# Kernel tuning notes

Hardware: AMD Instinct MI355X
Metric: run time of the kernel (lower is better)

## Reference

```python
import jax, jax.numpy as jnp
import numpy as np

N_NODES = 100000
N_EDGES = 1600000
IN_DIM, HID_DIM, OUT_DIM = 128, 256, 128


def gcn_conv(x, src, dst, W, b, n):
    # PyG GCNConv: linear transform, add self-loops, symmetric normalization,
    # scatter-sum aggregation over destination nodes, then bias.
    h = x @ W  # [n, d_out]
    loops = jnp.arange(n, dtype=src.dtype)
    s = jnp.concatenate([src, loops])
    d = jnp.concatenate([dst, loops])
    deg = jax.ops.segment_sum(jnp.ones_like(d, dtype=h.dtype), d, num_segments=n)
    dinv = jnp.where(deg > 0, jax.lax.rsqrt(deg), 0.0)
    norm = dinv[s] * dinv[d]  # [E+n]
    msg = h[s] * norm[:, None]  # gather + scale
    out = jax.ops.segment_sum(msg, d, num_segments=n)  # scatter-reduce
    return out + b


def layer_norm(x, gamma, beta, eps=1e-5):
    mu = jnp.mean(x, axis=-1, keepdims=True)
    var = jnp.mean(jnp.square(x - mu), axis=-1, keepdims=True)
    return (x - mu) * jax.lax.rsqrt(var + eps) * gamma + beta


def setup_inputs() -> dict:
    key = jax.random.key(0)
    ks = jax.random.split(key, 8)
    x = jax.random.normal(ks[0], (N_NODES, IN_DIM), dtype=jnp.float32)
    edge_index = jax.random.randint(ks[1], (2, N_EDGES), 0, N_NODES, dtype=jnp.int64)
    W1 = jax.random.normal(ks[2], (IN_DIM, HID_DIM), dtype=jnp.float32) * (1.0 / np.sqrt(IN_DIM))
    b1 = jnp.zeros((HID_DIM,), dtype=jnp.float32)
    W2 = jax.random.normal(ks[3], (HID_DIM, OUT_DIM), dtype=jnp.float32) * (1.0 / np.sqrt(HID_DIM))
    b2 = jnp.zeros((OUT_DIM,), dtype=jnp.float32)
    gamma = jnp.ones((OUT_DIM,), dtype=jnp.float32)
    beta = jnp.zeros((OUT_DIM,), dtype=jnp.float32)
    return {"x": x, "edge_index": edge_index, "W1": W1, "b1": b1,
            "W2": W2, "b2": b2, "gamma": gamma, "beta": beta}


def reference(x, edge_index, W1, b1, W2, b2, gamma, beta):
    n = x.shape[0]
    src, dst = edge_index[0], edge_index[1]
    h = gcn_conv(x, src, dst, W1, b1, n)
    h = jax.nn.relu(h)
    # dropout(p=0.1) is identity in eval mode
    h = gcn_conv(h, src, dst, W2, b2, n)
    return layer_norm(h, gamma, beta)
```

## Files before the change

kernel.cpp:

```cpp
#include <hip/hip_runtime.h>
#include <hip/hip_fp16.h>
#include <stdint.h>

#define N_NODES 100000
#define N_EDGES 1600000
#define IN_DIM  128
#define HID_DIM 256
#define OUT_DIM 128
#define RS 264
#define NBUCK 391
#define EPB   4096
#define PADB  5120
#define PB    391
#define WB    256

typedef __attribute__((ext_vector_type(8))) _Float16 f16x8;
typedef __attribute__((ext_vector_type(4))) float f32x4;

__device__ __forceinline__ int clampi(int v) {
    v = v < 0 ? 0 : v;
    return v >= N_NODES ? N_NODES - 1 : v;
}
__device__ __forceinline__ float2 h2f2(uint32_t u) {
    union { uint32_t u; __half2 h; } c; c.u = u;
    return __half22float2(c.h);
}
__device__ __forceinline__ uint32_t packh(float a, float b) {
    union { __half2 h; uint32_t u; } c; c.h = __floats2half2_rn(a, b);
    return c.u;
}
__device__ __forceinline__ uint16_t f2h(float a) {
    union { __half h; uint16_t s; } c; c.h = __float2half_rn(a);
    return c.s;
}

__device__ __forceinline__ int src_at(const int* ei, int isI64, int e) {
    return clampi(isI64 ? ei[2 * (size_t)e] : ei[e]);
}
__device__ __forceinline__ int dst_at(const int* ei, int isI64, int e) {
    return clampi(isI64 ? ei[2 * (size_t)N_EDGES + 2 * (size_t)e]
                        : ei[(size_t)N_EDGES + e]);
}


__global__ __launch_bounds__(256) void partition_kernel(const int* __restrict__ ei,
                                                        int* __restrict__ cursor,
                                                        uint2* __restrict__ recs,
                                                        const float* __restrict__ W1,
                                                        uint16_t* __restrict__ W1t,
                                                        const float* __restrict__ W2,
                                                        uint16_t* __restrict__ W2t) {
    if (blockIdx.x >= PB) {
        int idx = (blockIdx.x - PB) * 256 + threadIdx.x;
        if (idx < IN_DIM * HID_DIM) {
            int k = idx / HID_DIM, n = idx - k * HID_DIM;
            W1t[n * IN_DIM + k] = f2h(W1[idx]);
        } else {
            int j = idx - IN_DIM * HID_DIM;
            int k = j / OUT_DIM, n = j - k * OUT_DIM;
            W2t[n * HID_DIM + k] = f2h(W2[j]);
        }
        return;
    }
    __shared__ int hist[NBUCK];
    __shared__ int histBase[NBUCK];
    __shared__ int gBase[NBUCK];
    __shared__ int scanT[512];
    __shared__ uint2 lrec[EPB];
    __shared__ int s_flag;
    int tid = threadIdx.x;
    if (tid == 0) {
        int z = 1;
        #pragma unroll
        for (int i = 0; i < 16; ++i)
            if (ei[2 * i + 1] != 0) z = 0;
        s_flag = z;
    }
    for (int b = tid; b < NBUCK; b += 256) hist[b] = 0;
    __syncthreads();
    int isI64 = s_flag;
    int base = blockIdx.x * EPB;
    int srcs[16], dsts[16], slots[16];
    #pragma unroll
    for (int r = 0; r < 16; ++r) {
        int e = base + r * 256 + tid;
        slots[r] = -1;
        srcs[r] = 0; dsts[r] = 0;
        if (e < N_EDGES) {
            srcs[r] = src_at(ei, isI64, e);
            dsts[r] = dst_at(ei, isI64, e);
            slots[r] = atomicAdd(&hist[dsts[r] >> 8], 1);
        }
    }
    __syncthreads();
    scanT[tid]       = (tid < NBUCK) ? hist[tid] : 0;
    scanT[tid + 256] = (tid + 256 < NBUCK) ? hist[tid + 256] : 0;
    __syncthreads();
    for (int off = 1; off < 512; off <<= 1) {
        int v0 = (tid >= off) ? scanT[tid - off] : 0;
        int v1 = scanT[tid + 256 - off];
        __syncthreads();
        if (tid >= off) scanT[tid] += v0;
        scanT[tid + 256] += v1;
        __syncthreads();
    }
    for (int b = tid; b < NBUCK; b += 256) {
        histBase[b] = b ? scanT[b - 1] : 0;
        if (hist[b] > 0) gBase[b] = atomicAdd(&cursor[b], hist[b]);
    }
    __syncthreads();
    #pragma unroll
    for (int r = 0; r < 16; ++r) {
        if (slots[r] >= 0) {
            int b = dsts[r] >> 8;
            uint2 rec; rec.x = (unsigned)srcs[r]; rec.y = (unsigned)dsts[r];
            lrec[histBase[b] + slots[r]] = rec;
        }
    }
    __syncthreads();
    int nvalid = N_EDGES - base; if (nvalid > EPB) nvalid = EPB;
    for (int i = tid; i < nvalid; i += 256) {
        uint2 rec = lrec[i];
        int b = (int)(rec.y >> 8);
        int pos = gBase[b] + (i - histBase[b]);
        if (pos < PADB)
            recs[(size_t)b * PADB + pos] = rec;
    }
}


__global__ __launch_bounds__(256) void build_kernel(const uint2* __restrict__ recs,
                                                    const int* __restrict__ cursor,
                                                    int* __restrict__ row_ptr,
                                                    float* __restrict__ dinv,
                                                    int* __restrict__ colv,
                                                    const float* __restrict__ x,
                                                    uint2* __restrict__ xsout) {
    __shared__ uint2 lrec[PADB];
    __shared__ int cnt[256];
    __shared__ int lofs[256];
    __shared__ int cur[256];
    __shared__ int scanT[256];
    int b = blockIdx.x, tid = threadIdx.x;
    int nb = cursor[b]; if (nb > PADB) nb = PADB;
    int pv = 0;
    for (int j = tid; j < b; j += 256) {
        int c = cursor[j];
        pv += (c > PADB) ? PADB : c;
    }
    cnt[tid] = 0; cur[tid] = 0;
    scanT[tid] = pv;
    __syncthreads();
    for (int off = 128; off > 0; off >>= 1) {
        if (tid < off) scanT[tid] += scanT[tid + off];
        __syncthreads();
    }
    int cbase = scanT[0];
    __syncthreads();
    for (int i = tid; i < nb; i += 256) {
        uint2 r = recs[(size_t)b * PADB + i];
        lrec[i] = r;
        atomicAdd(&cnt[r.y & 255], 1);
    }
    __syncthreads();
    scanT[tid] = cnt[tid];
    __syncthreads();
    for (int off = 1; off < 256; off <<= 1) {
        int x2 = (tid >= off) ? scanT[tid - off] : 0;
        __syncthreads();
        if (tid >= off) scanT[tid] += x2;
        __syncthreads();
    }
    lofs[tid] = tid ? scanT[tid - 1] : 0;
    int node = b * 256 + tid;
    if (node < N_NODES) {
        row_ptr[node] = cbase + lofs[tid];
        dinv[node] = rsqrtf((float)(cnt[tid] + 1));
    }
    if (b == NBUCK - 1 && tid == 0) row_ptr[N_NODES] = cbase + nb;
    __syncthreads();
    for (int i = tid; i < nb; i += 256) {
        uint2 r = lrec[i];
        int id = (int)(r.y & 255);
        int slot = atomicAdd(&cur[id], 1);
        colv[cbase + lofs[id] + slot] = (int)r.x;
    }
    const float4* x4 = (const float4*)x + (size_t)b * 8192;
    uint2* xo = xsout + (size_t)b * 8192;
    int lim = (N_NODES - b * 256) * 32; if (lim > 8192) lim = 8192;
    for (int j = tid; j < lim; j += 256) {
        float d = rsqrtf((float)(cnt[j >> 5] + 1));
        float4 v = x4[j];
        uint2 o;
        o.x = packh(d * v.x, d * v.y);
        o.y = packh(d * v.z, d * v.w);
        xo[j] = o;
    }
}


template<bool LN>
__global__ __launch_bounds__(256) void agg_kernel(const uint4* __restrict__ rows,
                                                  const int* __restrict__ row_ptr,
                                                  const int* __restrict__ colv,
                                                  const float* __restrict__ dinv,
                                                  const float* __restrict__ bias,
                                                  const float* __restrict__ gamma,
                                                  const float* __restrict__ beta,
                                                  float* __restrict__ out,
                                                  uint4* __restrict__ out16) {
    int node = blockIdx.x * 16 + (threadIdx.x >> 4);
    if (node >= N_NODES) return;
    int l = threadIdx.x & 15;
    const char* base = (const char*)rows + ((unsigned)l << 4);
    float di = dinv[node];
    float acc[8];
    {
        uint4 u = *(const uint4*)(base + ((unsigned)node << 8));
        float2 f0 = h2f2(u.x), f1 = h2f2(u.y), f2 = h2f2(u.z), f3 = h2f2(u.w);
        acc[0] = f0.x; acc[1] = f0.y; acc[2] = f1.x; acc[3] = f1.y;
        acc[4] = f2.x; acc[5] = f2.y; acc[6] = f3.x; acc[7] = f3.y;
    }
    int e = row_ptr[node], e1 = row_ptr[node + 1];
    int s0 = 0, s1 = 0, s2 = 0, s3 = 0;
    if (e     < e1) s0 = colv[e];
    if (e + 1 < e1) s1 = colv[e + 1];
    if (e + 2 < e1) s2 = colv[e + 2];
    if (e + 3 < e1) s3 = colv[e + 3];
    while (e + 4 <= e1) {
        uint4 v0 = *(const uint4*)(base + ((unsigned)s0 << 8));
        uint4 v1 = *(const uint4*)(base + ((unsigned)s1 << 8));
        uint4 v2 = *(const uint4*)(base + ((unsigned)s2 << 8));
        uint4 v3 = *(const uint4*)(base + ((unsigned)s3 << 8));
        int p0 = (e + 4 < e1) ? e + 4 : e;
        int p1 = (e + 5 < e1) ? e + 5 : e;
        int p2 = (e + 6 < e1) ? e + 6 : e;
        int p3 = (e + 7 < e1) ? e + 7 : e;
        int t0 = colv[p0], t1 = colv[p1], t2 = colv[p2], t3 = colv[p3];
        {
            float2 f0 = h2f2(v0.x), f1 = h2f2(v0.y), f2 = h2f2(v0.z), f3 = h2f2(v0.w);
            acc[0] += f0.x; acc[1] += f0.y; acc[2] += f1.x; acc[3] += f1.y;
            acc[4] += f2.x; acc[5] += f2.y; acc[6] += f3.x; acc[7] += f3.y;
        }
        {
            float2 f0 = h2f2(v1.x), f1 = h2f2(v1.y), f2 = h2f2(v1.z), f3 = h2f2(v1.w);
            acc[0] += f0.x; acc[1] += f0.y; acc[2] += f1.x; acc[3] += f1.y;
            acc[4] += f2.x; acc[5] += f2.y; acc[6] += f3.x; acc[7] += f3.y;
        }
        {
            float2 f0 = h2f2(v2.x), f1 = h2f2(v2.y), f2 = h2f2(v2.z), f3 = h2f2(v2.w);
            acc[0] += f0.x; acc[1] += f0.y; acc[2] += f1.x; acc[3] += f1.y;
            acc[4] += f2.x; acc[5] += f2.y; acc[6] += f3.x; acc[7] += f3.y;
        }
        {
            float2 f0 = h2f2(v3.x), f1 = h2f2(v3.y), f2 = h2f2(v3.z), f3 = h2f2(v3.w);
            acc[0] += f0.x; acc[1] += f0.y; acc[2] += f1.x; acc[3] += f1.y;
            acc[4] += f2.x; acc[5] += f2.y; acc[6] += f3.x; acc[7] += f3.y;
        }
        s0 = t0; s1 = t1; s2 = t2; s3 = t3; e += 4;
    }
    int r = e1 - e;
    if (r > 0) {
        uint4 v = *(const uint4*)(base + ((unsigned)s0 << 8));
        float2 f0 = h2f2(v.x), f1 = h2f2(v.y), f2 = h2f2(v.z), f3 = h2f2(v.w);
        acc[0] += f0.x; acc[1] += f0.y; acc[2] += f1.x; acc[3] += f1.y;
        acc[4] += f2.x; acc[5] += f2.y; acc[6] += f3.x; acc[7] += f3.y;
    }
    if (r > 1) {
        uint4 v = *(const uint4*)(base + ((unsigned)s1 << 8));
        float2 f0 = h2f2(v.x), f1 = h2f2(v.y), f2 = h2f2(v.z), f3 = h2f2(v.w);
        acc[0] += f0.x; acc[1] += f0.y; acc[2] += f1.x; acc[3] += f1.y;
        acc[4] += f2.x; acc[5] += f2.y; acc[6] += f3.x; acc[7] += f3.y;
    }
    if (r > 2) {
        uint4 v = *(const uint4*)(base + ((unsigned)s2 << 8));
        float2 f0 = h2f2(v.x), f1 = h2f2(v.y), f2 = h2f2(v.z), f3 = h2f2(v.w);
        acc[0] += f0.x; acc[1] += f0.y; acc[2] += f1.x; acc[3] += f1.y;
        acc[4] += f2.x; acc[5] += f2.y; acc[6] += f3.x; acc[7] += f3.y;
    }
    if (!LN) {
        uint4 o;
        o.x = packh(acc[0] * di, acc[1] * di);
        o.y = packh(acc[2] * di, acc[3] * di);
        o.z = packh(acc[4] * di, acc[5] * di);
        o.w = packh(acc[6] * di, acc[7] * di);
        out16[(size_t)node * 16 + l] = o;
    } else {
        const float4* b4 = (const float4*)(bias + l * 8);
        float4 bb0 = b4[0], bb1 = b4[1];
        float v[8];
        v[0] = acc[0] * di + bb0.x; v[1] = acc[1] * di + bb0.y;
        v[2] = acc[2] * di + bb0.z; v[3] = acc[3] * di + bb0.w;
        v[4] = acc[4] * di + bb1.x; v[5] = acc[5] * di + bb1.y;
        v[6] = acc[6] * di + bb1.z; v[7] = acc[7] * di + bb1.w;
        float s = 0.f;
        #pragma unroll
        for (int j = 0; j < 8; ++j) s += v[j];
        #pragma unroll
        for (int o = 8; o > 0; o >>= 1) s += __shfl_xor(s, o, 64);
        float mu = s * (1.0f / 128.0f);
        float q = 0.f;
        #pragma unroll
        for (int j = 0; j < 8; ++j) { v[j] -= mu; q += v[j] * v[j]; }
        #pragma unroll
        for (int o = 8; o > 0; o >>= 1) q += __shfl_xor(q, o, 64);
        float rstd = rsqrtf(q * (1.0f / 128.0f) + 1e-5f);
        const float4* g4 = (const float4*)(gamma + l * 8);
        const float4* t4 = (const float4*)(beta + l * 8);
        float4 g0 = g4[0], g1 = g4[1], t0 = t4[0], t1 = t4[1];
        float* orow = out + (size_t)node * 128 + l * 8;
        f32x4 o0, o1;
        o0.x = v[0] * rstd * g0.x + t0.x; o0.y = v[1] * rstd * g0.y + t0.y;
        o0.z = v[2] * rstd * g0.z + t0.z; o0.w = v[3] * rstd * g0.w + t0.w;
        o1.x = v[4] * rstd * g1.x + t1.x; o1.y = v[5] * rstd * g1.y + t1.y;
        o1.z = v[6] * rstd * g1.z + t1.z; o1.w = v[7] * rstd * g1.w + t1.w;
        __builtin_nontemporal_store(o0, (f32x4*)orow);
        __builtin_nontemporal_store(o1, (f32x4*)(orow + 4));
    }
}


__global__ __launch_bounds__(256) void fused_gemm_kernel(const uint16_t* __restrict__ A16,
                                                         const uint16_t* __restrict__ W1t,
                                                         const float* __restrict__ b1,
                                                         const uint16_t* __restrict__ W2t,
                                                         const float* __restrict__ dinv,
                                                         uint16_t* __restrict__ G16, int M) {
    __shared__ __align__(16) uint16_t Hs[64 * RS];
    int lane = threadIdx.x & 63;
    int wave = threadIdx.x >> 6;
    int r15 = lane & 15;
    int quad = lane >> 4;
    int kofs = quad * 8;
    int blk_row = blockIdx.x * 64;

    f16x8 a[4][4];
    #pragma unroll
    for (int mt = 0; mt < 4; ++mt) {
        bool valid = (blk_row + mt * 16) < M;
        int row = valid ? (blk_row + mt * 16 + r15) : 0;
        const uint16_t* arow = A16 + (size_t)row * IN_DIM + kofs;
        #pragma unroll
        for (int ks = 0; ks < 4; ++ks)
            a[mt][ks] = *(const f16x8*)(arow + ks * 32);
    }

    #pragma unroll
    for (int nt = 0; nt < 4; ++nt) {
        int ncol = (wave * 4 + nt) * 16 + r15;
        const uint16_t* bp = W1t + (size_t)ncol * IN_DIM + kofs;
        f32x4 acc[4];
        #pragma unroll
        for (int mt = 0; mt < 4; ++mt) acc[mt] = (f32x4){0.f, 0.f, 0.f, 0.f};
        #pragma unroll
        for (int ks = 0; ks < 4; ++ks) {
            f16x8 bv = *(const f16x8*)(bp + ks * 32);
            #pragma unroll
            for (int mt = 0; mt < 4; ++mt)
                acc[mt] = __builtin_amdgcn_mfma_f32_16x16x32_f16(a[mt][ks], bv, acc[mt], 0, 0, 0);
        }
        float bb = b1[ncol];
        #pragma unroll
        for (int mt = 0; mt < 4; ++mt) {
            #pragma unroll
            for (int r = 0; r < 4; ++r) {
                int lrow = mt * 16 + quad * 4 + r;
                Hs[lrow * RS + ncol] = f2h(fmaxf(acc[mt][r] + bb, 0.f));
            }
        }
    }
    __syncthreads();

    #pragma unroll
    for (int nt = 0; nt < 2; ++nt) {
        int ncol = (wave * 2 + nt) * 16 + r15;
        const uint16_t* bp = W2t + (size_t)ncol * HID_DIM + kofs;
        f16x8 b2[8];
        #pragma unroll
        for (int ks = 0; ks < 8; ++ks)
            b2[ks] = *(const f16x8*)(bp + ks * 32);
        f32x4 acc[4];
        #pragma unroll
        for (int mt = 0; mt < 4; ++mt) acc[mt] = (f32x4){0.f, 0.f, 0.f, 0.f};
        #pragma unroll
        for (int ks = 0; ks < 8; ++ks) {
            #pragma unroll
            for (int mt = 0; mt < 4; ++mt) {
                f16x8 av = *(const f16x8*)(Hs + (mt * 16 + r15) * RS + ks * 32 + kofs);
                acc[mt] = __builtin_amdgcn_mfma_f32_16x16x32_f16(av, b2[ks], acc[mt], 0, 0, 0);
            }
        }
        #pragma unroll
        for (int mt = 0; mt < 4; ++mt) {
            if ((blk_row + mt * 16) < M) {
                #pragma unroll
                for (int r = 0; r < 4; ++r) {
                    int row = blk_row + mt * 16 + quad * 4 + r;
                    G16[(size_t)row * OUT_DIM + ncol] = f2h(dinv[row] * acc[mt][r]);
                }
            }
        }
    }
}


extern "C" void kernel_launch(void* const* d_in, const int* in_sizes, int n_in,
                              void* d_out, int out_size, void* d_ws, size_t ws_size,
                              hipStream_t stream) {
    const float* x     = (const float*)d_in[0];
    const int*   ei    = (const int*)d_in[1];
    const float* W1    = (const float*)d_in[2];
    const float* b1    = (const float*)d_in[3];
    const float* W2    = (const float*)d_in[4];
    const float* b2    = (const float*)d_in[5];
    const float* gamma = (const float*)d_in[6];
    const float* beta  = (const float*)d_in[7];

    char* ws = (char*)d_ws;
    size_t off = 0;
    auto alloc = [&](size_t bytes) -> void* {
        void* p = ws + off;
        off += (bytes + 511) & ~(size_t)511;
        return p;
    };
    int*      cursor  = (int*)alloc((size_t)NBUCK * 4);
    int*      row_ptr = (int*)alloc((size_t)(N_NODES + 1) * 4);
    float*    dinv    = (float*)alloc((size_t)N_NODES * 4);
    uint16_t* W1t     = (uint16_t*)alloc((size_t)IN_DIM * HID_DIM * 2);
    uint16_t* W2t     = (uint16_t*)alloc((size_t)HID_DIM * OUT_DIM * 2);
    int*      colv    = (int*)alloc((size_t)N_EDGES * 4);
    void*     big     = alloc((size_t)N_NODES * IN_DIM * 2);
    uint2*    recs    = (uint2*)big;
    uint16_t* g16     = (uint16_t*)big;
    if (ws_size < off) return;

    uint2*    xs16 = (uint2*)d_out;
    uint16_t* xa16 = (uint16_t*)d_out + (size_t)N_NODES * IN_DIM;

    const int AB = (N_NODES + 15) / 16;
    const int GB = (N_NODES + 63) / 64;

    hipMemsetAsync(cursor, 0, (size_t)NBUCK * 4, stream);
    partition_kernel<<<PB + WB, 256, 0, stream>>>(ei, cursor, recs, W1, W1t, W2, W2t);
    build_kernel<<<NBUCK, 256, 0, stream>>>(recs, cursor, row_ptr, dinv, colv, x, xs16);
    agg_kernel<false><<<AB, 256, 0, stream>>>((const uint4*)xs16, row_ptr, colv, dinv,
                                              nullptr, nullptr, nullptr,
                                              nullptr, (uint4*)xa16);
    fused_gemm_kernel<<<GB, 256, 0, stream>>>(xa16, W1t, b1, W2t, dinv, g16, N_NODES);
    agg_kernel<true><<<AB, 256, 0, stream>>>((const uint4*)g16, row_ptr, colv, dinv,
                                             b2, gamma, beta, (float*)d_out, nullptr);
}
```

Before: 328.4 us.

## Pack edge records into 32 bits and bucket CSR columns by source range

Edge records are packed into one 32-bit word (source<<8 | local destination) instead of an 8-byte pair, which halves the record traffic in the partition and build kernels. The bucket id is now found by a binary search over the shared scan array. The build kernel writes column indices in 13 passes grouped by the high bits of the source id, so each node's neighbour list comes out partly sorted by source. That ordering should give the aggregation gathers better cache locality. The cost is extra passes and barriers over shared memory in the build kernel, plus a per-element binary search in the partition kernel.

```diff
diff --git a/kernel.cpp b/kernel.cpp
--- a/kernel.cpp
+++ b/kernel.cpp
@@ -13,6 +13,8 @@
 #define PADB  5120
 #define PB    391
 #define WB    256
+#define CSH   13
+#define NCH   13
 
 typedef __attribute__((ext_vector_type(8))) _Float16 f16x8;
 typedef __attribute__((ext_vector_type(4))) float f32x4;
@@ -45,7 +47,7 @@
 
 __global__ __launch_bounds__(256) void partition_kernel(const int* __restrict__ ei,
                                                         int* __restrict__ cursor,
-                                                        uint2* __restrict__ recs,
+                                                        uint32_t* __restrict__ recs,
                                                         const float* __restrict__ W1,
                                                         uint16_t* __restrict__ W1t,
                                                         const float* __restrict__ W2,
@@ -66,7 +68,7 @@
     __shared__ int histBase[NBUCK];
     __shared__ int gBase[NBUCK];
     __shared__ int scanT[512];
-    __shared__ uint2 lrec[EPB];
+    __shared__ uint32_t lrec[EPB];
     __shared__ int s_flag;
     int tid = threadIdx.x;
     if (tid == 0) {
@@ -113,15 +115,20 @@
     for (int r = 0; r < 16; ++r) {
         if (slots[r] >= 0) {
             int b = dsts[r] >> 8;
-            uint2 rec; rec.x = (unsigned)srcs[r]; rec.y = (unsigned)dsts[r];
-            lrec[histBase[b] + slots[r]] = rec;
+            lrec[histBase[b] + slots[r]] =
+                ((uint32_t)srcs[r] << 8) | (uint32_t)(dsts[r] & 255);
         }
     }
     __syncthreads();
     int nvalid = N_EDGES - base; if (nvalid > EPB) nvalid = EPB;
     for (int i = tid; i < nvalid; i += 256) {
-        uint2 rec = lrec[i];
-        int b = (int)(rec.y >> 8);
+        uint32_t rec = lrec[i];
+        int lo = 0, hi = NBUCK - 1;
+        while (lo < hi) {
+            int mid = (lo + hi) >> 1;
+            if (scanT[mid] > i) hi = mid; else lo = mid + 1;
+        }
+        int b = lo;
         int pos = gBase[b] + (i - histBase[b]);
         if (pos < PADB)
             recs[(size_t)b * PADB + pos] = rec;
@@ -129,14 +136,14 @@
 }
 
 
-__global__ __launch_bounds__(256) void build_kernel(const uint2* __restrict__ recs,
+__global__ __launch_bounds__(256) void build_kernel(const uint32_t* __restrict__ recs,
                                                     const int* __restrict__ cursor,
                                                     int* __restrict__ row_ptr,
                                                     float* __restrict__ dinv,
                                                     int* __restrict__ colv,
                                                     const float* __restrict__ x,
                                                     uint2* __restrict__ xsout) {
-    __shared__ uint2 lrec[PADB];
+    __shared__ uint32_t lrec[PADB];
     __shared__ int cnt[256];
     __shared__ int lofs[256];
     __shared__ int cur[256];
@@ -158,9 +165,9 @@
     int cbase = scanT[0];
     __syncthreads();
     for (int i = tid; i < nb; i += 256) {
-        uint2 r = recs[(size_t)b * PADB + i];
+        uint32_t r = recs[(size_t)b * PADB + i];
         lrec[i] = r;
-        atomicAdd(&cnt[r.y & 255], 1);
+        atomicAdd(&cnt[r & 255], 1);
     }
     __syncthreads();
     scanT[tid] = cnt[tid];
@@ -179,11 +186,17 @@
     }
     if (b == NBUCK - 1 && tid == 0) row_ptr[N_NODES] = cbase + nb;
     __syncthreads();
-    for (int i = tid; i < nb; i += 256) {
-        uint2 r = lrec[i];
-        int id = (int)(r.y & 255);
-        int slot = atomicAdd(&cur[id], 1);
-        colv[cbase + lofs[id] + slot] = (int)r.x;
+    for (int c = 0; c < NCH; ++c) {
+        for (int i = tid; i < nb; i += 256) {
+            uint32_t r = lrec[i];
+            uint32_t s = r >> 8;
+            if ((s >> CSH) == (uint32_t)c) {
+                int id = (int)(r & 255);
+                int slot = atomicAdd(&cur[id], 1);
+                colv[cbase + lofs[id] + slot] = (int)s;
+            }
+        }
+        __syncthreads();
     }
     const float4* x4 = (const float4*)x + (size_t)b * 8192;
     uint2* xo = xsout + (size_t)b * 8192;
@@ -430,7 +443,7 @@
     uint16_t* W2t     = (uint16_t*)alloc((size_t)HID_DIM * OUT_DIM * 2);
     int*      colv    = (int*)alloc((size_t)N_EDGES * 4);
     void*     big     = alloc((size_t)N_NODES * IN_DIM * 2);
-    uint2*    recs    = (uint2*)big;
+    uint32_t* recs    = (uint32_t*)big;
     uint16_t* g16     = (uint16_t*)big;
     if (ws_size < off) return;
 
```

Result: slower. 352.1 us (+7.2%).
